# Kernel optimization log

Measured on AMD Instinct MI355X. Metric: run time of the kernel, lower is better.

Reference implementation:

```python
import jax, jax.numpy as jnp
import numpy as np

N = 100000
E = 1600000
D_IN = 64
D_OUT = 64


def setup_inputs() -> dict:
    key = jax.random.key(0)
    k1, k2, k3, k4 = jax.random.split(key, 4)
    x = jax.random.normal(k1, (N, D_IN), dtype=jnp.float32)
    edge_index = jax.random.randint(k2, (2, E), 0, N, dtype=jnp.int32)
    # nn.Linear(in, out): weight [out, in]; we store W as [in, out] for x @ W
    W = jax.random.normal(k3, (D_IN, D_OUT), dtype=jnp.float32) * (1.0 / np.sqrt(D_IN))
    b = jax.random.normal(k4, (D_OUT,), dtype=jnp.float32) * 0.01
    return {"x": x, "edge_index": edge_index, "W": W, "b": b}


def reference(x, edge_index, W, b):
    n = x.shape[0]
    src, tgt = edge_index[0], edge_index[1]
    # gather neighbor feats and scatter-add into source nodes: agg[src] += x[tgt]
    agg = jax.ops.segment_sum(x[tgt], src, num_segments=n)  # [N, D_in]
    # degree normalization: bincount(src) + eps
    counts = jax.ops.segment_sum(jnp.ones((src.shape[0],), dtype=x.dtype), src,
                                 num_segments=n) + 1e-6  # [N]
    agg = agg / counts[:, None]
    return agg @ W + b  # [N, D_out]
```

## Files before the change

### kernel.cpp

```cpp
#include <hip/hip_runtime.h>
#include <hip/hip_fp16.h>

#define D 64
#define NPB 32
#define LOGNPB 5
#define BCAPS 128
#define NSHARD 8
#define FCHUNK 8192
#define SORTCAP 1024

typedef int v4i __attribute__((ext_vector_type(4)));

__device__ __forceinline__ float bcast(float v, int k) {
    return __uint_as_float(__builtin_amdgcn_readlane(__float_as_uint(v), k));
}

__global__ __launch_bounds__(256, 2) void fused_partition_gemm(
    const int* __restrict__ src, const int* __restrict__ tgt,
    int* __restrict__ gcur, int* __restrict__ part,
    const float* __restrict__ x, const float* __restrict__ W,
    __half* __restrict__ y,
    int E, int nbuck, int fill_blocks, int N, int gemm_nwaves)
{
    extern __shared__ int hist[];
    int tid = threadIdx.x;

    if ((int)blockIdx.x < fill_blocks) {
        int xsh = blockIdx.x & (NSHARD - 1);
        int* mycur  = gcur + (size_t)xsh * nbuck;
        int* mypart = part + (size_t)xsh * nbuck * BCAPS;

        for (int i = tid; i < nbuck; i += 256) hist[i] = 0;
        __syncthreads();

        int base = blockIdx.x * FCHUNK;
        int end = base + FCHUNK < E ? base + FCHUNK : E;
        int nfull = (end - base) & ~7;

        for (int i = base + tid * 8; i + 8 <= end; i += 256 * 8) {
            v4i s0 = *(const v4i*)(src + i);
            v4i s1 = *(const v4i*)(src + i + 4);
            int ss[8] = {s0.x, s0.y, s0.z, s0.w, s1.x, s1.y, s1.z, s1.w};
            #pragma unroll
            for (int j = 0; j < 8; ++j)
                atomicAdd(&hist[ss[j] >> LOGNPB], 1);
        }
        for (int i = base + nfull + tid; i < end; i += 256)
            atomicAdd(&hist[src[i] >> LOGNPB], 1);
        __syncthreads();

        for (int bkt = tid; bkt < nbuck; bkt += 256) {
            int h = hist[bkt];
            hist[bkt] = h ? atomicAdd(&mycur[bkt], h) : 0;
        }
        __syncthreads();

        for (int i = base + tid * 8; i + 8 <= end; i += 256 * 8) {
            v4i s0 = *(const v4i*)(src + i);
            v4i s1 = *(const v4i*)(src + i + 4);
            v4i t0 = *(const v4i*)(tgt + i);
            v4i t1 = *(const v4i*)(tgt + i + 4);
            int ss[8] = {s0.x, s0.y, s0.z, s0.w, s1.x, s1.y, s1.z, s1.w};
            int tt[8] = {t0.x, t0.y, t0.z, t0.w, t1.x, t1.y, t1.z, t1.w};
            int pos[8], bk[8];
            #pragma unroll
            for (int j = 0; j < 8; ++j) {
                bk[j] = ss[j] >> LOGNPB;
                pos[j] = atomicAdd(&hist[bk[j]], 1);
            }
            #pragma unroll
            for (int j = 0; j < 8; ++j)
                if ((unsigned)pos[j] < BCAPS)
                    mypart[(size_t)bk[j] * BCAPS + pos[j]] =
                        ((ss[j] & (NPB - 1)) << 20) | tt[j];
        }
        for (int i = base + nfull + tid; i < end; i += 256) {
            int s = src[i], t = tgt[i];
            int b = s >> LOGNPB;
            int p = atomicAdd(&hist[b], 1);
            if ((unsigned)p < BCAPS)
                mypart[(size_t)b * BCAPS + p] = ((s & (NPB - 1)) << 20) | t;
        }
    } else {
        int lane = tid & 63;
        if ((int)blockIdx.x == fill_blocks && tid < D)
            y[(size_t)N * D + tid] = __float2half(0.0f);

        float wcol[D];
        #pragma unroll
        for (int k = 0; k < D; ++k)
            wcol[k] = W[k * D + lane];

        int gw = ((int)blockIdx.x - fill_blocks) * 4 + (tid >> 6);
        for (int n = gw * 4; n < N; n += gemm_nwaves * 4) {
            int i1 = n + 1 < N ? n + 1 : N - 1;
            int i2 = n + 2 < N ? n + 2 : N - 1;
            int i3 = n + 3 < N ? n + 3 : N - 1;
            float x0 = x[(size_t)n  * D + lane];
            float x1 = x[(size_t)i1 * D + lane];
            float x2 = x[(size_t)i2 * D + lane];
            float x3 = x[(size_t)i3 * D + lane];

            float o0 = 0, o1 = 0, o2 = 0, o3 = 0;
            #pragma unroll
            for (int k = 0; k < D; ++k) {
                float w = wcol[k];
                o0 += bcast(x0, k) * w;
                o1 += bcast(x1, k) * w;
                o2 += bcast(x2, k) * w;
                o3 += bcast(x3, k) * w;
            }
            y[(size_t)n * D + lane] = __float2half(o0);
            if (n + 1 < N) y[(size_t)(n + 1) * D + lane] = __float2half(o1);
            if (n + 2 < N) y[(size_t)(n + 2) * D + lane] = __float2half(o2);
            if (n + 3 < N) y[(size_t)(n + 3) * D + lane] = __float2half(o3);
        }
    }
}

__global__ __launch_bounds__(256) void bucket_gather(
    const __half* __restrict__ y, const int* __restrict__ gcur,
    const int* __restrict__ part, const float* __restrict__ bias_v,
    float* __restrict__ out, int N, int nbuck, int zrow)
{
    __shared__ int cnt_s[NPB];
    __shared__ int off_s[NPB];
    __shared__ int cur_s[NPB];
    __shared__ int segc[NSHARD];
    __shared__ __align__(16) int sortbuf[SORTCAP];
    int tid = threadIdx.x, wave = tid >> 6, lane = tid & 63;
    int bk = blockIdx.x;

    if (tid < NPB) cnt_s[tid] = 0;
    if (tid < NSHARD) {
        int c = gcur[(size_t)tid * nbuck + bk];
        segc[tid] = c > BCAPS ? BCAPS : c;
    }
    for (int i = tid; i < SORTCAP; i += 256) sortbuf[i] = zrow;
    __syncthreads();

    int half = tid >> 7;
    int hid  = tid & 127;

    for (int sh = 0; sh < NSHARD; sh += 2) {
        int c = segc[sh + half];
        if (hid < c) {
            int w = part[((size_t)(sh + half) * nbuck + bk) * BCAPS + hid];
            atomicAdd(&cnt_s[w >> 20], 1);
        }
    }
    __syncthreads();

    if (wave == 0) {
        int v = (lane < NPB) ? cnt_s[lane] : 0;
        int r = (v + 7) & ~7;
        int s = r;
        #pragma unroll
        for (int d = 1; d < NPB; d <<= 1) {
            int t = __shfl_up(s, d);
            if ((lane & (NPB - 1)) >= d) s += t;
        }
        if (lane < NPB) {
            off_s[lane] = s - r;
            cur_s[lane] = s - r;
        }
    }
    __syncthreads();

    for (int sh = 0; sh < NSHARD; sh += 2) {
        int c = segc[sh + half];
        if (hid < c) {
            int w = part[((size_t)(sh + half) * nbuck + bk) * BCAPS + hid];
            int p = atomicAdd(&cur_s[w >> 20], 1);
            if (p < SORTCAP) sortbuf[p] = w & 0xFFFFF;
        }
    }
    __syncthreads();

    float bias = bias_v[lane];
    for (int r = wave; r < NPB; r += 4) {
        int n = (bk << LOGNPB) + r;
        if (n >= N) break;
        int dg = cnt_s[r];
        int rdeg = (dg + 7) & ~7;
        int start = off_s[r];

        float a0 = 0, a1 = 0, a2 = 0, a3 = 0, a4 = 0, a5 = 0, a6 = 0, a7 = 0;
        for (int i = start; i < start + rdeg; i += 8) {
            int4 q0 = *(const int4*)&sortbuf[i];
            int4 q1 = *(const int4*)&sortbuf[i + 4];
            a0 += __half2float(y[(size_t)q0.x * D + lane]);
            a1 += __half2float(y[(size_t)q0.y * D + lane]);
            a2 += __half2float(y[(size_t)q0.z * D + lane]);
            a3 += __half2float(y[(size_t)q0.w * D + lane]);
            a4 += __half2float(y[(size_t)q1.x * D + lane]);
            a5 += __half2float(y[(size_t)q1.y * D + lane]);
            a6 += __half2float(y[(size_t)q1.z * D + lane]);
            a7 += __half2float(y[(size_t)q1.w * D + lane]);
        }
        float scale = 1.0f / ((float)dg + 1e-6f);
        float a = ((a0 + a1) + (a2 + a3)) + ((a4 + a5) + (a6 + a7));
        __builtin_nontemporal_store(a * scale + bias, &out[(size_t)n * D + lane]);
    }
}

extern "C" void kernel_launch(void* const* d_in, const int* in_sizes, int n_in,
                              void* d_out, int out_size, void* d_ws, size_t ws_size,
                              hipStream_t stream) {
    const float* x  = (const float*)d_in[0];
    const int*   ei = (const int*)d_in[1];
    const float* W  = (const float*)d_in[2];
    const float* b  = (const float*)d_in[3];
    float* out = (float*)d_out;

    int N = in_sizes[0] / D;
    int E = in_sizes[1] / 2;
    const int* src = ei;
    const int* tgt = ei + E;

    int nbuck = (N + NPB - 1) >> LOGNPB;

    int* gcur = (int*)d_ws;
    int* part = gcur + (size_t)NSHARD * nbuck;
    __half* y = (__half*)(part + (size_t)NSHARD * nbuck * BCAPS);

    hipMemsetAsync(gcur, 0, (size_t)NSHARD * nbuck * sizeof(int), stream);

    int fb = (E + FCHUNK - 1) / FCHUNK;
    const int gemm_blocks = 1024;
    fused_partition_gemm<<<fb + gemm_blocks, 256, nbuck * sizeof(int), stream>>>(
        src, tgt, gcur, part, x, W, y, E, nbuck, fb, N, gemm_blocks * 4);

    bucket_gather<<<nbuck, 256, 0, stream>>>(y, gcur, part, b, out, N, nbuck, N);
}
```

Before: 169.7 us.

## Stage bucket edges in LDS once, use 32-bit indexing, nontemporal src loads

The gather kernel now loads each bucket's partitioned edge words from global memory into a shared staging array once, then runs the count and scatter passes over that array instead of reading the partition buffer twice. SORTCAP is raised to 1280 to leave headroom for per-row padding. Address math throughout switches from size_t multiplies to 32-bit shifts and ORs to reduce VALU work, and the first read of src in the partition pass uses nontemporal loads. In exchange the gather kernel uses more LDS, which may lower occupancy, and 32-bit indexing assumes the buffers stay under 4G elements.

```diff
diff --git a/kernel.cpp b/kernel.cpp
--- a/kernel.cpp
+++ b/kernel.cpp
@@ -7,7 +7,8 @@
 #define BCAPS 128
 #define NSHARD 8
 #define FCHUNK 8192
-#define SORTCAP 1024
+#define STAGECAP 1024
+#define SORTCAP 1280
 
 typedef int v4i __attribute__((ext_vector_type(4)));
 
@@ -38,8 +39,8 @@
         int nfull = (end - base) & ~7;
 
         for (int i = base + tid * 8; i + 8 <= end; i += 256 * 8) {
-            v4i s0 = *(const v4i*)(src + i);
-            v4i s1 = *(const v4i*)(src + i + 4);
+            v4i s0 = __builtin_nontemporal_load((const v4i*)(src + i));
+            v4i s1 = __builtin_nontemporal_load((const v4i*)(src + i + 4));
             int ss[8] = {s0.x, s0.y, s0.z, s0.w, s1.x, s1.y, s1.z, s1.w};
             #pragma unroll
             for (int j = 0; j < 8; ++j)
@@ -71,7 +72,7 @@
             #pragma unroll
             for (int j = 0; j < 8; ++j)
                 if ((unsigned)pos[j] < BCAPS)
-                    mypart[(size_t)bk[j] * BCAPS + pos[j]] =
+                    mypart[(unsigned)(bk[j] * BCAPS + pos[j])] =
                         ((ss[j] & (NPB - 1)) << 20) | tt[j];
         }
         for (int i = base + nfull + tid; i < end; i += 256) {
@@ -79,12 +80,12 @@
             int b = s >> LOGNPB;
             int p = atomicAdd(&hist[b], 1);
             if ((unsigned)p < BCAPS)
-                mypart[(size_t)b * BCAPS + p] = ((s & (NPB - 1)) << 20) | t;
+                mypart[(unsigned)(b * BCAPS + p)] = ((s & (NPB - 1)) << 20) | t;
         }
     } else {
         int lane = tid & 63;
         if ((int)blockIdx.x == fill_blocks && tid < D)
-            y[(size_t)N * D + tid] = __float2half(0.0f);
+            y[(unsigned)(N * D + tid)] = __float2half(0.0f);
 
         float wcol[D];
         #pragma unroll
@@ -96,10 +97,10 @@
             int i1 = n + 1 < N ? n + 1 : N - 1;
             int i2 = n + 2 < N ? n + 2 : N - 1;
             int i3 = n + 3 < N ? n + 3 : N - 1;
-            float x0 = x[(size_t)n  * D + lane];
-            float x1 = x[(size_t)i1 * D + lane];
-            float x2 = x[(size_t)i2 * D + lane];
-            float x3 = x[(size_t)i3 * D + lane];
+            float x0 = x[((unsigned)n  << 6) | lane];
+            float x1 = x[((unsigned)i1 << 6) | lane];
+            float x2 = x[((unsigned)i2 << 6) | lane];
+            float x3 = x[((unsigned)i3 << 6) | lane];
 
             float o0 = 0, o1 = 0, o2 = 0, o3 = 0;
             #pragma unroll
@@ -110,10 +111,10 @@
                 o2 += bcast(x2, k) * w;
                 o3 += bcast(x3, k) * w;
             }
-            y[(size_t)n * D + lane] = __float2half(o0);
-            if (n + 1 < N) y[(size_t)(n + 1) * D + lane] = __float2half(o1);
-            if (n + 2 < N) y[(size_t)(n + 2) * D + lane] = __float2half(o2);
-            if (n + 3 < N) y[(size_t)(n + 3) * D + lane] = __float2half(o3);
+            y[((unsigned)n << 6) | lane] = __float2half(o0);
+            if (n + 1 < N) y[((unsigned)(n + 1) << 6) | lane] = __float2half(o1);
+            if (n + 2 < N) y[((unsigned)(n + 2) << 6) | lane] = __float2half(o2);
+            if (n + 3 < N) y[((unsigned)(n + 3) << 6) | lane] = __float2half(o3);
         }
     }
 }
@@ -127,6 +128,8 @@
     __shared__ int off_s[NPB];
     __shared__ int cur_s[NPB];
     __shared__ int segc[NSHARD];
+    __shared__ int segoff[NSHARD + 1];
+    __shared__ int stage[STAGECAP];
     __shared__ __align__(16) int sortbuf[SORTCAP];
     int tid = threadIdx.x, wave = tid >> 6, lane = tid & 63;
     int bk = blockIdx.x;
@@ -139,16 +142,30 @@
     for (int i = tid; i < SORTCAP; i += 256) sortbuf[i] = zrow;
     __syncthreads();
 
+    if (tid == 0) {
+        int acc = 0;
+        #pragma unroll
+        for (int sh = 0; sh < NSHARD; ++sh) { segoff[sh] = acc; acc += segc[sh]; }
+        segoff[NSHARD] = acc;
+    }
+    __syncthreads();
+
     int half = tid >> 7;
     int hid  = tid & 127;
 
+    #pragma unroll
     for (int sh = 0; sh < NSHARD; sh += 2) {
-        int c = segc[sh + half];
-        if (hid < c) {
-            int w = part[((size_t)(sh + half) * nbuck + bk) * BCAPS + hid];
-            atomicAdd(&cnt_s[w >> 20], 1);
-        }
-    }
+        int s2 = sh + half;
+        int c = segc[s2];
+        if (hid < c)
+            stage[segoff[s2] + hid] =
+                part[(unsigned)((s2 * nbuck + bk) * BCAPS + hid)];
+    }
+    __syncthreads();
+    int tot = segoff[NSHARD];
+
+    for (int i = tid; i < tot; i += 256)
+        atomicAdd(&cnt_s[stage[i] >> 20], 1);
     __syncthreads();
 
     if (wave == 0) {
@@ -167,13 +184,10 @@
     }
     __syncthreads();
 
-    for (int sh = 0; sh < NSHARD; sh += 2) {
-        int c = segc[sh + half];
-        if (hid < c) {
-            int w = part[((size_t)(sh + half) * nbuck + bk) * BCAPS + hid];
-            int p = atomicAdd(&cur_s[w >> 20], 1);
-            if (p < SORTCAP) sortbuf[p] = w & 0xFFFFF;
-        }
+    for (int i = tid; i < tot; i += 256) {
+        int w = stage[i];
+        int p = atomicAdd(&cur_s[w >> 20], 1);
+        if (p < SORTCAP) sortbuf[p] = w & 0xFFFFF;
     }
     __syncthreads();
 
@@ -189,18 +203,19 @@
         for (int i = start; i < start + rdeg; i += 8) {
             int4 q0 = *(const int4*)&sortbuf[i];
             int4 q1 = *(const int4*)&sortbuf[i + 4];
-            a0 += __half2float(y[(size_t)q0.x * D + lane]);
-            a1 += __half2float(y[(size_t)q0.y * D + lane]);
-            a2 += __half2float(y[(size_t)q0.z * D + lane]);
-            a3 += __half2float(y[(size_t)q0.w * D + lane]);
-            a4 += __half2float(y[(size_t)q1.x * D + lane]);
-            a5 += __half2float(y[(size_t)q1.y * D + lane]);
-            a6 += __half2float(y[(size_t)q1.z * D + lane]);
-            a7 += __half2float(y[(size_t)q1.w * D + lane]);
+            a0 += __half2float(y[((unsigned)q0.x << 6) | lane]);
+            a1 += __half2float(y[((unsigned)q0.y << 6) | lane]);
+            a2 += __half2float(y[((unsigned)q0.z << 6) | lane]);
+            a3 += __half2float(y[((unsigned)q0.w << 6) | lane]);
+            a4 += __half2float(y[((unsigned)q1.x << 6) | lane]);
+            a5 += __half2float(y[((unsigned)q1.y << 6) | lane]);
+            a6 += __half2float(y[((unsigned)q1.z << 6) | lane]);
+            a7 += __half2float(y[((unsigned)q1.w << 6) | lane]);
         }
         float scale = 1.0f / ((float)dg + 1e-6f);
         float a = ((a0 + a1) + (a2 + a3)) + ((a4 + a5) + (a6 + a7));
-        __builtin_nontemporal_store(a * scale + bias, &out[(size_t)n * D + lane]);
+        __builtin_nontemporal_store(a * scale + bias,
+                                    &out[((unsigned)n << 6) | lane]);
     }
 }
 
```

After: 169.2 us. About the same (-0.3%).
